# Performance work log

Hardware: AMD Instinct MI355X
Metric: run time of the kernel (lower is better)

Reference implementation:

```python
import jax, jax.numpy as jnp
import numpy as np

# Dimensions
B, D1, D2 = 256, 68, 3          # inputs: [B, 68 landmarks, 3 coords]
OUT = D1 * D2                   # output_size = 204
H = 1024                        # hidden_size
NUM_CLASSES = 12
LENGTH = 128                    # decoded sequence length
NUM_LAYERS = 3
IN0 = OUT + NUM_CLASSES         # LSTM layer-0 input size = 216


def setup_inputs() -> dict:
    key = jax.random.key(0)
    ks = jax.random.split(key, 32)
    s = 0.02

    def rn(k, shape):
        return (jax.random.normal(k, shape, jnp.float32) * s)

    inp = {
        "inputs": jax.random.normal(ks[0], (B, D1, D2), jnp.float32),
        # LSTM layer 0 (input size IN0), layers 1,2 (input size H). Gate order: i,f,g,o.
        "W_ih0": rn(ks[1], (IN0, 4 * H)), "W_hh0": rn(ks[2], (H, 4 * H)),
        "b_ih0": rn(ks[3], (4 * H,)),     "b_hh0": rn(ks[4], (4 * H,)),
        "W_ih1": rn(ks[5], (H, 4 * H)),   "W_hh1": rn(ks[6], (H, 4 * H)),
        "b_ih1": rn(ks[7], (4 * H,)),     "b_hh1": rn(ks[8], (4 * H,)),
        "W_ih2": rn(ks[9], (H, 4 * H)),   "W_hh2": rn(ks[10], (H, 4 * H)),
        "b_ih2": rn(ks[11], (4 * H,)),    "b_hh2": rn(ks[12], (4 * H,)),
        # fc head: hidden -> output_size
        "fc_W": rn(ks[13], (H, OUT)), "fc_b": rn(ks[14], (OUT,)),
        # state initializers: output_size -> 3*hidden
        "inh_W": rn(ks[15], (OUT, 3 * H)), "inh_b": rn(ks[16], (3 * H,)),
        "inc_W": rn(ks[17], (OUT, 3 * H)), "inc_b": rn(ks[18], (3 * H,)),
        "labels": 5,  # scalar class id
    }
    return inp


def _lstm_cell(x, h, c, W_ih, W_hh, b_ih, b_hh):
    gates = x @ W_ih + h @ W_hh + (b_ih + b_hh)        # [B, 4H]
    i, f, g, o = jnp.split(gates, 4, axis=-1)
    i = jax.nn.sigmoid(i)
    f = jax.nn.sigmoid(f)
    g = jnp.tanh(g)
    o = jax.nn.sigmoid(o)
    c2 = f * c + i * g
    h2 = o * jnp.tanh(c2)
    return h2, c2


def reference(inputs, W_ih0, W_hh0, b_ih0, b_hh0,
              W_ih1, W_hh1, b_ih1, b_hh1,
              W_ih2, W_hh2, b_ih2, b_hh2,
              fc_W, fc_b, inh_W, inh_b, inc_W, inc_b, labels):
    b, d1, d2 = inputs.shape
    frame = inputs.reshape(b, d1 * d2)                              # [B, OUT]
    # init states, reshaped (B, 3, H) -> (layers, B, H)
    h0 = (frame @ inh_W + inh_b).reshape(b, NUM_LAYERS, H).transpose(1, 0, 2)
    c0 = (frame @ inc_W + inc_b).reshape(b, NUM_LAYERS, H).transpose(1, 0, 2)
    enc = jax.nn.one_hot(jnp.asarray(labels), NUM_CLASSES, dtype=frame.dtype)
    x_in = jnp.concatenate([frame, jnp.broadcast_to(enc, (b, NUM_CLASSES))], axis=-1)  # [B, IN0]

    layers = ((W_ih0, W_hh0, b_ih0, b_hh0),
              (W_ih1, W_hh1, b_ih1, b_hh1),
              (W_ih2, W_hh2, b_ih2, b_hh2))

    def step(carry, _):
        h, c = carry                                                # each [3, B, H]
        x = x_in
        hs, cs = [], []
        for l in range(NUM_LAYERS):
            hn, cn = _lstm_cell(x, h[l], c[l], *layers[l])
            hs.append(hn)
            cs.append(cn)
            x = hn
        out = x @ fc_W + fc_b                                       # [B, OUT]
        return (jnp.stack(hs), jnp.stack(cs)), out

    (_, _), outs = jax.lax.scan(step, (h0, c0), None, length=LENGTH)  # [L, B, OUT]
    return outs.transpose(1, 0, 2).reshape(b, LENGTH, d1, d2)
```

## Files before the change

kernel.cpp:

```cpp
#include <hip/hip_runtime.h>


#define DEVINL static __device__ __forceinline__

typedef __bf16 bf16x8 __attribute__((ext_vector_type(8)));
typedef float f32x4 __attribute__((ext_vector_type(4)));
typedef unsigned short u16;
typedef unsigned int u32;
typedef unsigned long long u64;

DEVINL u16 f2bf(float f) {
  u32 u = __builtin_bit_cast(u32, f);
  u += 0x7fffu + ((u >> 16) & 1u);
  return (u16)(u >> 16);
}
DEVINL float bf2f(u16 h) {
  u32 u = (u32)h << 16;
  return __builtin_bit_cast(float, u);
}
DEVINL float sigm(float x) { return 1.0f / (1.0f + __expf(-x)); }
DEVINL float tanhfast(float x) { return 1.0f - 2.0f / (1.0f + __expf(2.0f * x)); }

DEVINL void glds_coh(const u16* g, u16* l) {
  __builtin_amdgcn_global_load_lds(
      (const __attribute__((address_space(1))) u32*)g,
      (__attribute__((address_space(3))) u32*)l, 16, 0, 17);
}
DEVINL void glds_w(const u16* g, u16* l) {
  __builtin_amdgcn_global_load_lds(
      (const __attribute__((address_space(1))) u32*)g,
      (__attribute__((address_space(3))) u32*)l, 16, 0, 0);
}

DEVINL int permcol(int P) {
  int grp = P >> 6, g = (P >> 4) & 3, jj = P & 15;
  return g * 1024 + grp * 16 + jj;
}

struct Params {
  const float* fc_b;
  const float* inh_b;
  const float* inc_b;
  const u16 *WT0, *WT1, *WT2, *WT00, *FCW, *WIH, *WIC, *FRB;
  u16* HB;
  u16* G0P;
  float *G0B, *B1P, *B2P, *CC;
  float* out;
};

#define MODE_L0 0
#define MODE_L 1
#define MODE_FC 2
#define MODE_G0 3
#define MODE_H 4
#define MODE_C 5

DEVINL void issue_tile(int kt, const u16* A0, const u16* A1, int kSplit, int sA,
                       int K, const u16* Wt, int m0, int wrow,
                       const int (&rq)[4], const int (&kqs)[4],
                       const int (&lo)[4], u16* Abuf, u16* Bbuf) {
  const u16* Ab = (kt < kSplit) ? (A0 + kt) : (A1 + (kt - kSplit));
#pragma unroll
  for (int q = 0; q < 4; ++q)
    glds_coh(Ab + (size_t)(m0 + rq[q]) * sA + kqs[q] * 8, Abuf + lo[q]);
  const u16* Bb = Wt + kt;
#pragma unroll
  for (int q = 0; q < 2; ++q)
    glds_w(Bb + (size_t)(wrow + rq[q]) * K + kqs[q] * 8, Bbuf + lo[q]);
}

DEVINL void mfma_tile(const u16* Al, const u16* Bl, f32x4 (&acc)[2][4], int rl0,
                      int hh, int e7, int jj) {
#pragma unroll
  for (int kk = 0; kk < 2; ++kk) {
    int sl = (((kk << 2) | hh) ^ e7) * 8;
    bf16x8 a0 = *(const bf16x8*)(Al + rl0 * 64 + sl);
    bf16x8 a1 = *(const bf16x8*)(Al + (rl0 + 16) * 64 + sl);
    bf16x8 b0 = *(const bf16x8*)(Bl + (jj)*64 + sl);
    bf16x8 b1 = *(const bf16x8*)(Bl + (16 + jj) * 64 + sl);
    bf16x8 b2 = *(const bf16x8*)(Bl + (32 + jj) * 64 + sl);
    bf16x8 b3 = *(const bf16x8*)(Bl + (48 + jj) * 64 + sl);
    acc[0][0] = __builtin_amdgcn_mfma_f32_16x16x32_bf16(a0, b0, acc[0][0], 0, 0, 0);
    acc[0][1] = __builtin_amdgcn_mfma_f32_16x16x32_bf16(a0, b1, acc[0][1], 0, 0, 0);
    acc[0][2] = __builtin_amdgcn_mfma_f32_16x16x32_bf16(a0, b2, acc[0][2], 0, 0, 0);
    acc[0][3] = __builtin_amdgcn_mfma_f32_16x16x32_bf16(a0, b3, acc[0][3], 0, 0, 0);
    acc[1][0] = __builtin_amdgcn_mfma_f32_16x16x32_bf16(a1, b0, acc[1][0], 0, 0, 0);
    acc[1][1] = __builtin_amdgcn_mfma_f32_16x16x32_bf16(a1, b1, acc[1][1], 0, 0, 0);
    acc[1][2] = __builtin_amdgcn_mfma_f32_16x16x32_bf16(a1, b2, acc[1][2], 0, 0, 0);
    acc[1][3] = __builtin_amdgcn_mfma_f32_16x16x32_bf16(a1, b3, acc[1][3], 0, 0, 0);
  }
}

template <int MODE>
DEVINL void mm_body(u16* Al, u16* Bl, const u16* A0, const u16* A1, int sA,
                    int kSplit, int K, const u16* Wt, int m0, int bn, int t,
                    const u16* Gfull, const float* biasP, float* Cst, u16* Hout,
                    float* outp) {
  const int tid = threadIdx.x;
  const int l = tid & 63;
  const int w = tid >> 6;
  const int hh = (l >> 4) & 3;
  const int jj = l & 15;
  const int rl0 = w * 32 + jj;
  const int e7 = l & 7;

  int rq[4], kqs[4], lo[4];
#pragma unroll
  for (int q = 0; q < 4; ++q) {
    int L = tid + q * 256;
    rq[q] = L >> 3;
    kqs[q] = (L & 7) ^ (rq[q] & 7);
    lo[q] = ((tid & ~63) + q * 256) * 8;
  }

  f32x4 acc[2][4];
#pragma unroll
  for (int m = 0; m < 2; ++m)
#pragma unroll
    for (int g = 0; g < 4; ++g) acc[m][g] = (f32x4){0.f, 0.f, 0.f, 0.f};

  const int wrow = bn * 64;
  const int n = K >> 6;

  issue_tile(0, A0, A1, kSplit, sA, K, Wt, m0, wrow, rq, kqs, lo, Al, Bl);
  issue_tile(64, A0, A1, kSplit, sA, K, Wt, m0, wrow, rq, kqs, lo, Al + 8192,
             Bl + 4096);

  for (int j = 0; j < n; ++j) {
    u16* Ac = Al + (j & 1) * 8192;
    u16* Bc = Bl + (j & 1) * 4096;
    if (j < n - 1)
      asm volatile("s_waitcnt vmcnt(6)" ::: "memory");
    else
      asm volatile("s_waitcnt vmcnt(0)" ::: "memory");
    __builtin_amdgcn_s_barrier();
    __builtin_amdgcn_sched_barrier(0);
    mfma_tile(Ac, Bc, acc, rl0, hh, e7, jj);
    __builtin_amdgcn_sched_barrier(0);
    __builtin_amdgcn_s_barrier();
    if (j + 2 < n)
      issue_tile((j + 2) * 64, A0, A1, kSplit, sA, K, Wt, m0, wrow, rq, kqs, lo,
                 Ac, Bc);
  }

  const int rb = m0 + w * 32 + (hh << 2);
  if (MODE <= MODE_L) {
    float add0 = 0.f, add1 = 0.f, add2 = 0.f, add3 = 0.f;
    if (MODE == MODE_L) {
      add0 = biasP[bn * 64 + jj];
      add1 = biasP[bn * 64 + 16 + jj];
      add2 = biasP[bn * 64 + 32 + jj];
      add3 = biasP[bn * 64 + 48 + jj];
    }
    const int j = bn * 16 + jj;
#pragma unroll
    for (int m = 0; m < 2; ++m) {
#pragma unroll
      for (int r = 0; r < 4; ++r) {
        int b = rb + m * 16 + r;
        float g0v, g1v, g2v, g3v;
        if (MODE == MODE_L0) {
          const u16* G = Gfull + (size_t)b * 4096 + bn * 64 + jj;
          g0v = acc[m][0][r] + bf2f(G[0]);
          g1v = acc[m][1][r] + bf2f(G[16]);
          g2v = acc[m][2][r] + bf2f(G[32]);
          g3v = acc[m][3][r] + bf2f(G[48]);
        } else {
          g0v = acc[m][0][r] + add0;
          g1v = acc[m][1][r] + add1;
          g2v = acc[m][2][r] + add2;
          g3v = acc[m][3][r] + add3;
        }
        float iv = sigm(g0v), fv = sigm(g1v), gv = tanhfast(g2v), ov = sigm(g3v);
        size_t ci = (size_t)b * 1024 + j;
        float cn = fv * Cst[ci] + iv * gv;
        Cst[ci] = cn;
        Hout[ci] = f2bf(ov * tanhfast(cn));
      }
    }
  } else if (MODE == MODE_FC) {
#pragma unroll
    for (int g = 0; g < 4; ++g) {
      int nn = bn * 64 + g * 16 + jj;
      if (nn < 204) {
        float bv2 = biasP[nn];
#pragma unroll
        for (int m = 0; m < 2; ++m)
#pragma unroll
          for (int r = 0; r < 4; ++r) {
            int b = rb + m * 16 + r;
            outp[((size_t)b * 128 + t) * 204 + nn] = acc[m][g][r] + bv2;
          }
      }
    }
  } else if (MODE == MODE_G0) {
#pragma unroll
    for (int g = 0; g < 4; ++g) {
      int P = bn * 64 + g * 16 + jj;
      float bv2 = biasP[P];
#pragma unroll
      for (int m = 0; m < 2; ++m)
#pragma unroll
        for (int r = 0; r < 4; ++r) {
          int b = rb + m * 16 + r;
          Hout[(size_t)b * 4096 + P] = f2bf(acc[m][g][r] + bv2);
        }
    }
  } else {
#pragma unroll
    for (int g = 0; g < 4; ++g) {
      int nn = bn * 64 + g * 16 + jj;
      int lay = nn >> 10, j2 = nn & 1023;
      float bv2 = biasP[nn];
#pragma unroll
      for (int m = 0; m < 2; ++m)
#pragma unroll
        for (int r = 0; r < 4; ++r) {
          int b = rb + m * 16 + r;
          float v = acc[m][g][r] + bv2;
          if (MODE == MODE_H)
            Hout[(size_t)((lay * 2 + 1) * 256 + b) * 1024 + j2] = f2bf(v);
          else
            outp[(size_t)(lay * 256 + b) * 1024 + j2] = v;
        }
    }
  }
}


DEVINL void step_barrier(u32* bar, int bid, int x, int rank, int nb, int ep) {
  __syncthreads();
  const int tid = threadIdx.x;
  if (tid == 0) {
    __hip_atomic_fetch_add(bar + 2048 + x * 64, 1u, __ATOMIC_RELAXED,
                           __HIP_MEMORY_SCOPE_AGENT);
    if (rank == 0) {
#pragma unroll 1
      while (__hip_atomic_load(bar + 2048 + x * 64, __ATOMIC_RELAXED,
                               __HIP_MEMORY_SCOPE_AGENT) < (u32)ep * (u32)nb)
        __builtin_amdgcn_s_sleep(4);
      __builtin_amdgcn_fence(__ATOMIC_RELEASE, "agent");
      __hip_atomic_fetch_add(bar + x * 64, 1u, __ATOMIC_RELAXED,
                             __HIP_MEMORY_SCOPE_AGENT);
    }
  }
  if (bid == 0) {
    if (tid < 8) {
      u32 cnt = __hip_atomic_load(bar + 1024 + tid * 64, __ATOMIC_RELAXED,
                                  __HIP_MEMORY_SCOPE_AGENT);
      if (cnt > 0) {
#pragma unroll 1
        while (__hip_atomic_load(bar + tid * 64, __ATOMIC_RELAXED,
                                 __HIP_MEMORY_SCOPE_AGENT) < (u32)ep)
          __builtin_amdgcn_s_sleep(4);
      }
    }
    __syncthreads();
    if (tid == 0)
      __hip_atomic_store(bar + 512, (u32)ep, __ATOMIC_RELAXED,
                         __HIP_MEMORY_SCOPE_AGENT);
  } else if (tid == 0) {
#pragma unroll 1
    while (__hip_atomic_load(bar + 512, __ATOMIC_RELAXED,
                             __HIP_MEMORY_SCOPE_AGENT) < (u32)ep)
      __builtin_amdgcn_s_sleep(8);
  }
  __syncthreads();
}

__global__ __launch_bounds__(256, 2) void persist_kernel(Params p, u32* bar) {
  __shared__ u16 Al[2 * 128 * 64];
  __shared__ u16 Bl[2 * 64 * 64];
  __shared__ int sh_x, sh_rank, sh_nb;
  const int bid = blockIdx.x;
  int job, mb, bn;
  if (bid < 384) {
    job = bid >> 7;
    int r = bid & 127;
    bn = (r & 7) * 8 + (r >> 4);
    mb = (r >> 3) & 1;
  } else {
    job = 3;
    int r = bid - 384;
    mb = r >> 2;
    bn = r & 3;
  }

  if (threadIdx.x == 0) {
    int x = __builtin_amdgcn_s_getreg((31 << 11) | 20) & 7;
    sh_x = x;
    sh_rank = (int)__hip_atomic_fetch_add(bar + 1024 + x * 64, 1u,
                                          __ATOMIC_RELAXED,
                                          __HIP_MEMORY_SCOPE_AGENT);
  }
  __syncthreads();
  const int x = sh_x, rank = sh_rank;
  if (threadIdx.x == 0) {
    __hip_atomic_fetch_add(bar + 768, 1u, __ATOMIC_RELAXED,
                           __HIP_MEMORY_SCOPE_AGENT);
#pragma unroll 1
    while (__hip_atomic_load(bar + 768, __ATOMIC_RELAXED,
                             __HIP_MEMORY_SCOPE_AGENT) < 392u)
      __builtin_amdgcn_s_sleep(8);
    sh_nb = (int)__hip_atomic_load(bar + 1024 + x * 64, __ATOMIC_RELAXED,
                                   __HIP_MEMORY_SCOPE_AGENT);
  }
  __syncthreads();
  const int nb = sh_nb;

  u16* HB = p.HB;
#define HBP(lay, pp) (HB + (size_t)(((lay)*2 + (pp)) << 18))
  for (int i = 0; i <= 130; ++i) {
    int t = i - job;
    if ((unsigned)t < 128u) {
      int par = t & 1, pv = par ^ 1;
      if (job == 0) {
        mm_body<MODE_L0>(Al, Bl, HBP(0, pv), nullptr, 1024, 1 << 30, 1024,
                         p.WT0, mb * 128, bn, t, p.G0P, nullptr, p.CC,
                         HBP(0, par), nullptr);
      } else if (job == 1) {
        mm_body<MODE_L>(Al, Bl, HBP(0, par), HBP(1, pv), 1024, 1024, 2048,
                        p.WT1, mb * 128, bn, t, nullptr, p.B1P,
                        p.CC + (size_t)256 * 1024, HBP(1, par), nullptr);
      } else if (job == 2) {
        mm_body<MODE_L>(Al, Bl, HBP(1, par), HBP(2, pv), 1024, 1024, 2048,
                        p.WT2, mb * 128, bn, t, nullptr, p.B2P,
                        p.CC + (size_t)512 * 1024, HBP(2, par), nullptr);
      } else {
        mm_body<MODE_FC>(Al, Bl, HBP(2, par), nullptr, 1024, 1 << 30, 1024,
                         p.FCW, mb * 128, bn, t, nullptr, p.fc_b, nullptr,
                         nullptr, p.out);
      }
    }
    if (i < 130) step_barrier(bar, bid, x, rank, nb, i + 1);
  }
#undef HBP
}

__global__ __launch_bounds__(256, 2) void setup_mm(Params p) {
  __shared__ u16 Al[2 * 128 * 64];
  __shared__ u16 Bl[2 * 64 * 64];
  int bid = blockIdx.x;
  if (bid < 128) {
    mm_body<MODE_G0>(Al, Bl, p.FRB, nullptr, 256, 1 << 30, 256, p.WT00,
                     (bid >> 6) * 128, bid & 63, 0, nullptr, p.G0B, nullptr,
                     p.G0P, nullptr);
  } else if (bid < 224) {
    int b2 = bid - 128;
    mm_body<MODE_H>(Al, Bl, p.FRB, nullptr, 256, 1 << 30, 256, p.WIH,
                    (b2 / 48) * 128, b2 % 48, 0, nullptr, p.inh_b, nullptr,
                    p.HB, nullptr);
  } else {
    int b2 = bid - 224;
    mm_body<MODE_C>(Al, Bl, p.FRB, nullptr, 256, 1 << 30, 256, p.WIC,
                    (b2 / 48) * 128, b2 % 48, 0, nullptr, p.inc_b, nullptr,
                    nullptr, p.CC);
  }
}

__global__ __launch_bounds__(256) void transpose_bf16(
    const float* __restrict__ srcA, const float* __restrict__ srcB,
    int srcStride, int kSplit, int Kvalid, int Nvalid, int perm,
    u16* __restrict__ dst, int Ktot) {
  __shared__ float tile[64][17];
  int P0 = blockIdx.x * 16;
  int k0 = blockIdx.y * 64;
  int t = threadIdx.x;
  int nl = t & 15;
  int kh = t >> 4;
  int P = P0 + nl;
  int n = perm ? permcol(P) : P;
  bool nok = (n < Nvalid);
#pragma unroll
  for (int q = 0; q < 4; ++q) {
    int kl = q * 16 + kh;
    int k = k0 + kl;
    float v = 0.f;
    if (nok && k < Kvalid) {
      const float* s = (k < kSplit) ? (srcA + (size_t)k * srcStride)
                                    : (srcB + (size_t)(k - kSplit) * srcStride);
      v = s[n];
    }
    tile[kl][nl] = v;
  }
  __syncthreads();
  int jo = t >> 4;
  int kb = (t & 15) << 2;
  u64 pk = (u64)f2bf(tile[kb + 0][jo]) | ((u64)f2bf(tile[kb + 1][jo]) << 16) |
           ((u64)f2bf(tile[kb + 2][jo]) << 32) |
           ((u64)f2bf(tile[kb + 3][jo]) << 48);
  *(u64*)(dst + (size_t)(P0 + jo) * Ktot + k0 + kb) = pk;
}

__global__ __launch_bounds__(256) void build_frame(const float* __restrict__ inputs,
                                                   u16* __restrict__ FRB) {
  int id = blockIdx.x * 256 + threadIdx.x;
  int b = id >> 8, k = id & 255;
  FRB[id] = (k < 204) ? f2bf(inputs[b * 204 + k]) : (u16)0;
}

__global__ __launch_bounds__(256) void build_bias(
    const float* __restrict__ W_ih0, const float* __restrict__ b_ih0,
    const float* __restrict__ b_hh0, const float* __restrict__ b_ih1,
    const float* __restrict__ b_hh1, const float* __restrict__ b_ih2,
    const float* __restrict__ b_hh2, const int* __restrict__ labels,
    float* __restrict__ G0B, float* __restrict__ B1P, float* __restrict__ B2P) {
  int P = blockIdx.x * 256 + threadIdx.x;
  int n = permcol(P);
  int lab = labels[0];
  G0B[P] = W_ih0[(size_t)(204 + lab) * 4096 + n] + b_ih0[n] + b_hh0[n];
  B1P[P] = b_ih1[n] + b_hh1[n];
  B2P[P] = b_ih2[n] + b_hh2[n];
}

extern "C" void kernel_launch(void* const* d_in, const int* in_sizes, int n_in,
                              void* d_out, int out_size, void* d_ws,
                              size_t ws_size, hipStream_t stream) {
  const float* inputs = (const float*)d_in[0];
  const float* W_ih0 = (const float*)d_in[1];
  const float* W_hh0 = (const float*)d_in[2];
  const float* b_ih0 = (const float*)d_in[3];
  const float* b_hh0 = (const float*)d_in[4];
  const float* W_ih1 = (const float*)d_in[5];
  const float* W_hh1 = (const float*)d_in[6];
  const float* b_ih1 = (const float*)d_in[7];
  const float* b_hh1 = (const float*)d_in[8];
  const float* W_ih2 = (const float*)d_in[9];
  const float* W_hh2 = (const float*)d_in[10];
  const float* b_ih2 = (const float*)d_in[11];
  const float* b_hh2 = (const float*)d_in[12];
  const float* fc_W = (const float*)d_in[13];
  const float* fc_b = (const float*)d_in[14];
  const float* inh_W = (const float*)d_in[15];
  const float* inh_b = (const float*)d_in[16];
  const float* inc_W = (const float*)d_in[17];
  const float* inc_b = (const float*)d_in[18];
  const int* labels = (const int*)d_in[19];

  char* ws = (char*)d_ws;
  size_t off = 0;
  auto alloc = [&](size_t bytes) {
    void* r = ws + off;
    off = (off + bytes + 255) & ~(size_t)255;
    return r;
  };
  u16* WT0 = (u16*)alloc(4096ull * 1024 * 2);
  u16* WT1 = (u16*)alloc(4096ull * 2048 * 2);
  u16* WT2 = (u16*)alloc(4096ull * 2048 * 2);
  u16* WT00 = (u16*)alloc(4096ull * 256 * 2);
  u16* FCW = (u16*)alloc(256ull * 1024 * 2);
  u16* WIH = (u16*)alloc(3072ull * 256 * 2);
  u16* WIC = (u16*)alloc(3072ull * 256 * 2);
  u16* FRB = (u16*)alloc(256ull * 256 * 2);
  u16* HB = (u16*)alloc(3ull * 2 * 256 * 1024 * 2);
  u16* G0P = (u16*)alloc(256ull * 4096 * 2);
  float* G0B = (float*)alloc(4096ull * 4);
  float* B1P = (float*)alloc(4096ull * 4);
  float* B2P = (float*)alloc(4096ull * 4);
  float* CC = (float*)alloc(3ull * 256 * 1024 * 4);
  u32* BAR = (u32*)alloc(16384);
  if (off > ws_size) return;

  const int BIG = 1 << 30;
  transpose_bf16<<<dim3(256, 16), 256, 0, stream>>>(W_hh0, nullptr, 4096, BIG, 1024, 4096, 1, WT0, 1024);
  transpose_bf16<<<dim3(256, 32), 256, 0, stream>>>(W_ih1, W_hh1, 4096, 1024, 2048, 4096, 1, WT1, 2048);
  transpose_bf16<<<dim3(256, 32), 256, 0, stream>>>(W_ih2, W_hh2, 4096, 1024, 2048, 4096, 1, WT2, 2048);
  transpose_bf16<<<dim3(256, 4), 256, 0, stream>>>(W_ih0, nullptr, 4096, BIG, 204, 4096, 1, WT00, 256);
  transpose_bf16<<<dim3(16, 16), 256, 0, stream>>>(fc_W, nullptr, 204, BIG, 1024, 204, 0, FCW, 1024);
  transpose_bf16<<<dim3(192, 4), 256, 0, stream>>>(inh_W, nullptr, 3072, BIG, 204, 3072, 0, WIH, 256);
  transpose_bf16<<<dim3(192, 4), 256, 0, stream>>>(inc_W, nullptr, 3072, BIG, 204, 3072, 0, WIC, 256);
  build_frame<<<256, 256, 0, stream>>>(inputs, FRB);
  build_bias<<<16, 256, 0, stream>>>(W_ih0, b_ih0, b_hh0, b_ih1, b_hh1, b_ih2,
                                     b_hh2, labels, G0B, B1P, B2P);
  hipMemsetAsync(BAR, 0, 16384, stream);

  Params p;
  p.fc_b = fc_b; p.inh_b = inh_b; p.inc_b = inc_b;
  p.WT0 = WT0; p.WT1 = WT1; p.WT2 = WT2; p.WT00 = WT00; p.FCW = FCW;
  p.WIH = WIH; p.WIC = WIC; p.FRB = FRB; p.HB = HB;
  p.G0P = G0P; p.G0B = G0B; p.B1P = B1P; p.B2P = B2P; p.CC = CC;
  p.out = (float*)d_out;

  setup_mm<<<320, 256, 0, stream>>>(p);

  persist_kernel<<<392, 256, 0, stream>>>(p, BAR);
}
```

Before: 4.299 ms.

## Reshape GEMM tiles to 64x256 with 512-thread blocks, halving persistent block count

Changes the per-block GEMM tile from 128 rows x 64 gate columns to 64 rows x 256 columns, with 8 waves per block arranged 2x4, and launches 512-thread blocks. The persistent kernel drops from 392 to 196 blocks and setup_mm from 320 to 160. Fewer blocks means fewer participants in the per-step grid barrier, and each block reuses its A tile across more weight columns. In exchange each block streams more weight data per step, and the FC job now uses one block per 64 rows with most columns padded.

New measurement: 5.274 ms. 22.7% more time.

```diff
diff --git a/kernel.cpp b/kernel.cpp
--- a/kernel.cpp
+++ b/kernel.cpp
@@ -55,31 +55,32 @@
 #define MODE_H 4
 #define MODE_C 5
 
+#define ASLOT 4096
+#define BSLOT 16384
+
 DEVINL void issue_tile(int kt, const u16* A0, const u16* A1, int kSplit, int sA,
-                       int K, const u16* Wt, int m0, int wrow,
-                       const int (&rq)[4], const int (&kqs)[4],
-                       const int (&lo)[4], u16* Abuf, u16* Bbuf) {
+                       int K, const u16* Wt, int m0, int wrow, int rqA, int kqA,
+                       int loA, const int (&rqB)[4], const int (&kqB)[4],
+                       const int (&loB)[4], u16* Abuf, u16* Bbuf) {
   const u16* Ab = (kt < kSplit) ? (A0 + kt) : (A1 + (kt - kSplit));
+  glds_coh(Ab + (size_t)(m0 + rqA) * sA + kqA * 8, Abuf + loA);
+  const u16* Bb = Wt + kt;
 #pragma unroll
   for (int q = 0; q < 4; ++q)
-    glds_coh(Ab + (size_t)(m0 + rq[q]) * sA + kqs[q] * 8, Abuf + lo[q]);
-  const u16* Bb = Wt + kt;
-#pragma unroll
-  for (int q = 0; q < 2; ++q)
-    glds_w(Bb + (size_t)(wrow + rq[q]) * K + kqs[q] * 8, Bbuf + lo[q]);
+    glds_w(Bb + (size_t)(wrow + rqB[q]) * K + kqB[q] * 8, Bbuf + loB[q]);
 }
 
 DEVINL void mfma_tile(const u16* Al, const u16* Bl, f32x4 (&acc)[2][4], int rl0,
-                      int hh, int e7, int jj) {
+                      int nb0, int hh, int e7) {
 #pragma unroll
   for (int kk = 0; kk < 2; ++kk) {
     int sl = (((kk << 2) | hh) ^ e7) * 8;
     bf16x8 a0 = *(const bf16x8*)(Al + rl0 * 64 + sl);
     bf16x8 a1 = *(const bf16x8*)(Al + (rl0 + 16) * 64 + sl);
-    bf16x8 b0 = *(const bf16x8*)(Bl + (jj)*64 + sl);
-    bf16x8 b1 = *(const bf16x8*)(Bl + (16 + jj) * 64 + sl);
-    bf16x8 b2 = *(const bf16x8*)(Bl + (32 + jj) * 64 + sl);
-    bf16x8 b3 = *(const bf16x8*)(Bl + (48 + jj) * 64 + sl);
+    bf16x8 b0 = *(const bf16x8*)(Bl + (nb0)*64 + sl);
+    bf16x8 b1 = *(const bf16x8*)(Bl + (nb0 + 16) * 64 + sl);
+    bf16x8 b2 = *(const bf16x8*)(Bl + (nb0 + 32) * 64 + sl);
+    bf16x8 b3 = *(const bf16x8*)(Bl + (nb0 + 48) * 64 + sl);
     acc[0][0] = __builtin_amdgcn_mfma_f32_16x16x32_bf16(a0, b0, acc[0][0], 0, 0, 0);
     acc[0][1] = __builtin_amdgcn_mfma_f32_16x16x32_bf16(a0, b1, acc[0][1], 0, 0, 0);
     acc[0][2] = __builtin_amdgcn_mfma_f32_16x16x32_bf16(a0, b2, acc[0][2], 0, 0, 0);
@@ -101,16 +102,20 @@
   const int w = tid >> 6;
   const int hh = (l >> 4) & 3;
   const int jj = l & 15;
-  const int rl0 = w * 32 + jj;
+  const int rl0 = (w & 1) * 32 + jj;
+  const int nb0 = (w >> 1) * 64 + jj;
   const int e7 = l & 7;
 
-  int rq[4], kqs[4], lo[4];
+  const int rqA = tid >> 3;
+  const int kqA = (tid & 7) ^ (rqA & 7);
+  const int loA = (tid & ~63) * 8;
+  int rqB[4], kqB[4], loB[4];
 #pragma unroll
   for (int q = 0; q < 4; ++q) {
-    int L = tid + q * 256;
-    rq[q] = L >> 3;
-    kqs[q] = (L & 7) ^ (rq[q] & 7);
-    lo[q] = ((tid & ~63) + q * 256) * 8;
+    int L = tid + q * 512;
+    rqB[q] = L >> 3;
+    kqB[q] = (L & 7) ^ (rqB[q] & 7);
+    loB[q] = ((tid & ~63) + q * 512) * 8;
   }
 
   f32x4 acc[2][4];
@@ -119,40 +124,42 @@
 #pragma unroll
     for (int g = 0; g < 4; ++g) acc[m][g] = (f32x4){0.f, 0.f, 0.f, 0.f};
 
-  const int wrow = bn * 64;
-  const int n = K >> 6;
-
-  issue_tile(0, A0, A1, kSplit, sA, K, Wt, m0, wrow, rq, kqs, lo, Al, Bl);
-  issue_tile(64, A0, A1, kSplit, sA, K, Wt, m0, wrow, rq, kqs, lo, Al + 8192,
-             Bl + 4096);
-
-  for (int j = 0; j < n; ++j) {
-    u16* Ac = Al + (j & 1) * 8192;
-    u16* Bc = Bl + (j & 1) * 4096;
-    if (j < n - 1)
-      asm volatile("s_waitcnt vmcnt(6)" ::: "memory");
+  const int wrow = bn * 256;
+  const int nt = K >> 6;
+
+  issue_tile(0, A0, A1, kSplit, sA, K, Wt, m0, wrow, rqA, kqA, loA, rqB, kqB,
+             loB, Al, Bl);
+  issue_tile(64, A0, A1, kSplit, sA, K, Wt, m0, wrow, rqA, kqA, loA, rqB, kqB,
+             loB, Al + ASLOT, Bl + BSLOT);
+
+  for (int j = 0; j < nt; ++j) {
+    u16* Ac = Al + (j & 1) * ASLOT;
+    u16* Bc = Bl + (j & 1) * BSLOT;
+    if (j < nt - 1)
+      asm volatile("s_waitcnt vmcnt(5)" ::: "memory");
     else
       asm volatile("s_waitcnt vmcnt(0)" ::: "memory");
     __builtin_amdgcn_s_barrier();
     __builtin_amdgcn_sched_barrier(0);
-    mfma_tile(Ac, Bc, acc, rl0, hh, e7, jj);
+    mfma_tile(Ac, Bc, acc, rl0, nb0, hh, e7);
     __builtin_amdgcn_sched_barrier(0);
     __builtin_amdgcn_s_barrier();
-    if (j + 2 < n)
-      issue_tile((j + 2) * 64, A0, A1, kSplit, sA, K, Wt, m0, wrow, rq, kqs, lo,
-                 Ac, Bc);
-  }
-
-  const int rb = m0 + w * 32 + (hh << 2);
+    if (j + 2 < nt)
+      issue_tile((j + 2) * 64, A0, A1, kSplit, sA, K, Wt, m0, wrow, rqA, kqA,
+                 loA, rqB, kqB, loB, Ac, Bc);
+  }
+
+  const int rb = m0 + (w & 1) * 32 + (hh << 2);
+  const int nb = bn * 256 + (w >> 1) * 64;
   if (MODE <= MODE_L) {
     float add0 = 0.f, add1 = 0.f, add2 = 0.f, add3 = 0.f;
     if (MODE == MODE_L) {
-      add0 = biasP[bn * 64 + jj];
-      add1 = biasP[bn * 64 + 16 + jj];
-      add2 = biasP[bn * 64 + 32 + jj];
-      add3 = biasP[bn * 64 + 48 + jj];
-    }
-    const int j = bn * 16 + jj;
+      add0 = biasP[nb + jj];
+      add1 = biasP[nb + 16 + jj];
+      add2 = biasP[nb + 32 + jj];
+      add3 = biasP[nb + 48 + jj];
+    }
+    const int j = (nb >> 6) * 16 + jj;
 #pragma unroll
     for (int m = 0; m < 2; ++m) {
 #pragma unroll
@@ -160,7 +167,7 @@
         int b = rb + m * 16 + r;
         float g0v, g1v, g2v, g3v;
         if (MODE == MODE_L0) {
-          const u16* G = Gfull + (size_t)b * 4096 + bn * 64 + jj;
+          const u16* G = Gfull + (size_t)b * 4096 + nb + jj;
           g0v = acc[m][0][r] + bf2f(G[0]);
           g1v = acc[m][1][r] + bf2f(G[16]);
           g2v = acc[m][2][r] + bf2f(G[32]);
@@ -181,7 +188,7 @@
   } else if (MODE == MODE_FC) {
 #pragma unroll
     for (int g = 0; g < 4; ++g) {
-      int nn = bn * 64 + g * 16 + jj;
+      int nn = nb + g * 16 + jj;
       if (nn < 204) {
         float bv2 = biasP[nn];
 #pragma unroll
@@ -196,7 +203,7 @@
   } else if (MODE == MODE_G0) {
 #pragma unroll
     for (int g = 0; g < 4; ++g) {
-      int P = bn * 64 + g * 16 + jj;
+      int P = nb + g * 16 + jj;
       float bv2 = biasP[P];
 #pragma unroll
       for (int m = 0; m < 2; ++m)
@@ -209,7 +216,7 @@
   } else {
 #pragma unroll
     for (int g = 0; g < 4; ++g) {
-      int nn = bn * 64 + g * 16 + jj;
+      int nn = nb + g * 16 + jj;
       int lay = nn >> 10, j2 = nn & 1023;
       float bv2 = biasP[nn];
 #pragma unroll
@@ -268,22 +275,21 @@
   __syncthreads();
 }
 
-__global__ __launch_bounds__(256, 2) void persist_kernel(Params p, u32* bar) {
-  __shared__ u16 Al[2 * 128 * 64];
-  __shared__ u16 Bl[2 * 64 * 64];
+__global__ __launch_bounds__(512, 2) void persist_kernel(Params p, u32* bar) {
+  __shared__ u16 Al[2 * ASLOT];
+  __shared__ u16 Bl[2 * BSLOT];
   __shared__ int sh_x, sh_rank, sh_nb;
   const int bid = blockIdx.x;
   int job, mb, bn;
-  if (bid < 384) {
-    job = bid >> 7;
-    int r = bid & 127;
-    bn = (r & 7) * 8 + (r >> 4);
-    mb = (r >> 3) & 1;
+  if (bid < 192) {
+    job = bid >> 6;
+    int r = bid & 63;
+    bn = (r & 7) * 2 + (r >> 5);
+    mb = (r >> 3) & 3;
   } else {
     job = 3;
-    int r = bid - 384;
-    mb = r >> 2;
-    bn = r & 3;
+    mb = bid - 192;
+    bn = 0;
   }
 
   if (threadIdx.x == 0) {
@@ -300,7 +306,7 @@
                            __HIP_MEMORY_SCOPE_AGENT);
 #pragma unroll 1
     while (__hip_atomic_load(bar + 768, __ATOMIC_RELAXED,
-                             __HIP_MEMORY_SCOPE_AGENT) < 392u)
+                             __HIP_MEMORY_SCOPE_AGENT) < 196u)
       __builtin_amdgcn_s_sleep(8);
     sh_nb = (int)__hip_atomic_load(bar + 1024 + x * 64, __ATOMIC_RELAXED,
                                    __HIP_MEMORY_SCOPE_AGENT);
@@ -316,19 +322,19 @@
       int par = t & 1, pv = par ^ 1;
       if (job == 0) {
         mm_body<MODE_L0>(Al, Bl, HBP(0, pv), nullptr, 1024, 1 << 30, 1024,
-                         p.WT0, mb * 128, bn, t, p.G0P, nullptr, p.CC,
+                         p.WT0, mb * 64, bn, t, p.G0P, nullptr, p.CC,
                          HBP(0, par), nullptr);
       } else if (job == 1) {
         mm_body<MODE_L>(Al, Bl, HBP(0, par), HBP(1, pv), 1024, 1024, 2048,
-                        p.WT1, mb * 128, bn, t, nullptr, p.B1P,
+                        p.WT1, mb * 64, bn, t, nullptr, p.B1P,
                         p.CC + (size_t)256 * 1024, HBP(1, par), nullptr);
       } else if (job == 2) {
         mm_body<MODE_L>(Al, Bl, HBP(1, par), HBP(2, pv), 1024, 1024, 2048,
-                        p.WT2, mb * 128, bn, t, nullptr, p.B2P,
+                        p.WT2, mb * 64, bn, t, nullptr, p.B2P,
                         p.CC + (size_t)512 * 1024, HBP(2, par), nullptr);
       } else {
         mm_body<MODE_FC>(Al, Bl, HBP(2, par), nullptr, 1024, 1 << 30, 1024,
-                         p.FCW, mb * 128, bn, t, nullptr, p.fc_b, nullptr,
+                         p.FCW, mb * 64, bn, t, nullptr, p.fc_b, nullptr,
                          nullptr, p.out);
       }
     }
@@ -337,23 +343,23 @@
 #undef HBP
 }
 
-__global__ __launch_bounds__(256, 2) void setup_mm(Params p) {
-  __shared__ u16 Al[2 * 128 * 64];
-  __shared__ u16 Bl[2 * 64 * 64];
+__global__ __launch_bounds__(512, 2) void setup_mm(Params p) {
+  __shared__ u16 Al[2 * ASLOT];
+  __shared__ u16 Bl[2 * BSLOT];
   int bid = blockIdx.x;
-  if (bid < 128) {
+  if (bid < 64) {
     mm_body<MODE_G0>(Al, Bl, p.FRB, nullptr, 256, 1 << 30, 256, p.WT00,
-                     (bid >> 6) * 128, bid & 63, 0, nullptr, p.G0B, nullptr,
+                     (bid >> 4) * 64, bid & 15, 0, nullptr, p.G0B, nullptr,
                      p.G0P, nullptr);
-  } else if (bid < 224) {
-    int b2 = bid - 128;
+  } else if (bid < 112) {
+    int r = bid - 64;
     mm_body<MODE_H>(Al, Bl, p.FRB, nullptr, 256, 1 << 30, 256, p.WIH,
-                    (b2 / 48) * 128, b2 % 48, 0, nullptr, p.inh_b, nullptr,
-                    p.HB, nullptr);
+                    (r / 12) * 64, r % 12, 0, nullptr, p.inh_b, nullptr, p.HB,
+                    nullptr);
   } else {
-    int b2 = bid - 224;
+    int r = bid - 112;
     mm_body<MODE_C>(Al, Bl, p.FRB, nullptr, 256, 1 << 30, 256, p.WIC,
-                    (b2 / 48) * 128, b2 % 48, 0, nullptr, p.inc_b, nullptr,
+                    (r / 12) * 64, r % 12, 0, nullptr, p.inc_b, nullptr,
                     nullptr, p.CC);
   }
 }
@@ -481,7 +487,7 @@
   p.G0P = G0P; p.G0B = G0B; p.B1P = B1P; p.B2P = B2P; p.CC = CC;
   p.out = (float*)d_out;
 
-  setup_mm<<<320, 256, 0, stream>>>(p);
-
-  persist_kernel<<<392, 256, 0, stream>>>(p, BAR);
-}
+  setup_mm<<<160, 512, 0, stream>>>(p);
+
+  persist_kernel<<<196, 512, 0, stream>>>(p, BAR);
+}
```
